# Optimization experiments

Hardware: AMD Instinct MI355X
Metric: run time of the kernel (lower is better)

The kernel has to match this reference:

```python
import jax, jax.numpy as jnp
import numpy as np

N_HEAD = 16

def setup_inputs() -> dict:
    key = jax.random.key(0)
    k1, k2, k3, k4, k5 = jax.random.split(key, 5)
    B, T, C = 2, 2048, 1024
    scale = 1.0 / np.sqrt(C)
    return {
        "x": jax.random.normal(k1, (B, T, C), dtype=jnp.float32),
        "Wqkv": jax.random.normal(k2, (C, 3 * C), dtype=jnp.float32) * scale,
        "bqkv": jax.random.normal(k3, (3 * C,), dtype=jnp.float32) * 0.02,
        "Wproj": jax.random.normal(k4, (C, C), dtype=jnp.float32) * scale,
        "bproj": jax.random.normal(k5, (C,), dtype=jnp.float32) * 0.02,
    }

def reference(x, Wqkv, bqkv, Wproj, bproj):
    B, T, C = x.shape
    H = N_HEAD
    D = C // H
    # qkv projection, split last dim as (3, H, D): first C cols = q, etc.
    qkv = (x @ Wqkv + bqkv).reshape(B, T, 3, H, D)
    q, k, v = qkv[:, :, 0], qkv[:, :, 1], qkv[:, :, 2]  # (B, T, H, D)
    att = jnp.einsum("bqhd,bkhd->bhqk", q, k) * (1.0 / np.sqrt(D))
    causal = jnp.tril(jnp.ones((T, T), dtype=bool))
    att = jnp.where(causal, att, -jnp.inf)
    att = jax.nn.softmax(att, axis=-1)
    y = jnp.einsum("bhqk,bkhd->bqhd", att, v).reshape(B, T, C)
    return y @ Wproj + bproj
```

## Files before the change

kernel.cpp:

```cpp
#include <hip/hip_runtime.h>
#include <hip/hip_bf16.h>
#include <stdint.h>

typedef unsigned short u16;
typedef __attribute__((ext_vector_type(8))) short bf16x8;
typedef __attribute__((ext_vector_type(4))) float f32x4;

#define MFMA16(a,b,c) __builtin_amdgcn_mfma_f32_16x16x32_bf16((a),(b),(c),0,0,0)

__device__ __forceinline__ u16 f2bf(float f) {
    union { float f; uint32_t u; } v; v.f = f;
    return (u16)((v.u + 0x7FFFu + ((v.u >> 16) & 1u)) >> 16);
}

__global__ void k_convert(const float* __restrict__ in, u16* __restrict__ out) {
    int i = (blockIdx.x * 256 + threadIdx.x) * 4;
    f32x4 v = *(const f32x4*)(in + i);
    uint64_t p = (uint64_t)f2bf(v[0]) | ((uint64_t)f2bf(v[1]) << 16)
               | ((uint64_t)f2bf(v[2]) << 32) | ((uint64_t)f2bf(v[3]) << 48);
    *(uint64_t*)(out + i) = p;
}

__global__ void k_transpose_convert(const float* __restrict__ W, u16* __restrict__ WT,
                                    int R, int NC) {
    int id = blockIdx.x * 256 + threadIdx.x;
    int n = id % NC, kc = id / NC;
    bf16x8 o;
#pragma unroll
    for (int i = 0; i < 8; ++i)
        o[i] = (short)f2bf(W[(size_t)(kc * 8 + i) * NC + n]);
    *(bf16x8*)(WT + (size_t)n * R + kc * 8) = o;
}

__global__ void k_transpose_v(const u16* __restrict__ V, u16* __restrict__ Vt) {
    int id = blockIdx.x * 256 + threadIdx.x;
    int d = id & 63, tc = (id >> 6) & 255, bh = id >> 14;
    const u16* src = V + (size_t)bh * 131072 + d;
    u16* dst = Vt + (size_t)bh * 131072 + (size_t)d * 2048 + tc * 8;
    bf16x8 o;
#pragma unroll
    for (int i = 0; i < 8; ++i) o[i] = (short)src[(size_t)(tc * 8 + i) * 64];
    *(bf16x8*)dst = o;
}

template<int NREP, int MODE>
__device__ __forceinline__ void gemm_body(
    const u16* __restrict__ A, const u16* __restrict__ Bt,
    const float* __restrict__ bias,
    u16* __restrict__ outQKV, float* __restrict__ outF,
    int M, int N, int K)
{
    constexpr int BN = 32 * NREP;
    constexpr int WN = 16 * NREP;
    constexpr int BSLOTS = NREP / 2;
    __shared__ __align__(16) u16 As[2][128 * 32];
    __shared__ __align__(16) u16 Bs[2][BN * 32];
    const int tid = threadIdx.x;
    const int nbx = N / BN;
    const int bm = blockIdx.x / nbx, bn = blockIdx.x % nbx;
    const int m0 = bm << 7, n0 = bn * BN;
    const int l = tid & 63, w = tid >> 6;
    const int wr = w >> 1, wc = w & 1;
    const int kl = l >> 4, lr = l & 15;

    const u16* Ag = A + (size_t)m0 * K;
    const u16* Bg = Bt + (size_t)n0 * K;

    int a_src[2], a_dst[2];
#pragma unroll
    for (int s = 0; s < 2; ++s) {
        int cb = w * 128 + s * 64;
        int c = cb + l;
        int r = c >> 2, kc = c & 3;
        a_src[s] = r * K + ((kc ^ ((r >> 1) & 3)) << 3);
        a_dst[s] = cb << 3;
    }
    int b_src[BSLOTS], b_dst[BSLOTS];
#pragma unroll
    for (int s = 0; s < BSLOTS; ++s) {
        int cb = (w * BSLOTS + s) * 64;
        int c = cb + l;
        int r = c >> 2, kc = c & 3;
        b_src[s] = r * K + ((kc ^ ((r >> 1) & 3)) << 3);
        b_dst[s] = cb << 3;
    }

    int ra[4], rb[NREP];
#pragma unroll
    for (int m = 0; m < 4; ++m) {
        int row = wr * 64 + m * 16 + lr;
        ra[m] = row * 32 + (((kl ^ (row >> 1)) & 3) << 3);
    }
#pragma unroll
    for (int n = 0; n < NREP; ++n) {
        int row = wc * WN + n * 16 + lr;
        rb[n] = row * 32 + (((kl ^ (row >> 1)) & 3) << 3);
    }

    f32x4 acc[4][NREP] = {};

#pragma unroll
    for (int s = 0; s < 2; ++s)
        __builtin_amdgcn_global_load_lds(Ag + a_src[s], &As[0][a_dst[s]], 16, 0, 0);
#pragma unroll
    for (int s = 0; s < BSLOTS; ++s)
        __builtin_amdgcn_global_load_lds(Bg + b_src[s], &Bs[0][b_dst[s]], 16, 0, 0);
    __syncthreads();

    const int nK = K >> 5;
    int cur = 0;
    for (int ks = 0; ks < nK; ++ks) {
        if (ks + 1 < nK) {
            int off = (ks + 1) << 5;
#pragma unroll
            for (int s = 0; s < 2; ++s)
                __builtin_amdgcn_global_load_lds(Ag + a_src[s] + off,
                                                 &As[cur ^ 1][a_dst[s]], 16, 0, 0);
#pragma unroll
            for (int s = 0; s < BSLOTS; ++s)
                __builtin_amdgcn_global_load_lds(Bg + b_src[s] + off,
                                                 &Bs[cur ^ 1][b_dst[s]], 16, 0, 0);
        }
        bf16x8 af[4], bfr[NREP];
#pragma unroll
        for (int m = 0; m < 4; ++m) af[m] = *(const bf16x8*)&As[cur][ra[m]];
#pragma unroll
        for (int n = 0; n < NREP; ++n) bfr[n] = *(const bf16x8*)&Bs[cur][rb[n]];
#pragma unroll
        for (int m = 0; m < 4; ++m)
#pragma unroll
            for (int n = 0; n < NREP; ++n)
                acc[m][n] = MFMA16(af[m], bfr[n], acc[m][n]);
        __syncthreads();
        cur ^= 1;
    }

    if (MODE == 0) {
#pragma unroll
        for (int n = 0; n < NREP; ++n) {
            int gn = n0 + wc * WN + n * 16 + lr;
            float bv = bias[gn];
            int s = gn >> 10, hd = gn & 1023;
            int hh = hd >> 6, dd = hd & 63;
            float mult = (s == 0) ? 0.125f : 1.0f;
            size_t base = (size_t)s * 4194304 + (size_t)hh * 131072 + dd;
#pragma unroll
            for (int m = 0; m < 4; ++m)
#pragma unroll
                for (int j = 0; j < 4; ++j) {
                    int gm = m0 + wr * 64 + m * 16 + kl * 4 + j;
                    int bb = gm >> 11, tt = gm & 2047;
                    float val = (acc[m][n][j] + bv) * mult;
                    outQKV[base + (size_t)bb * 2097152 + (size_t)tt * 64] = f2bf(val);
                }
        }
    } else {
#pragma unroll
        for (int n = 0; n < NREP; ++n) {
            int gn = n0 + wc * WN + n * 16 + lr;
            float bv = bias[gn];
#pragma unroll
            for (int m = 0; m < 4; ++m)
#pragma unroll
                for (int j = 0; j < 4; ++j) {
                    int gm = m0 + wr * 64 + m * 16 + kl * 4 + j;
                    outF[(size_t)gm * N + gn] = acc[m][n][j] + bv;
                }
        }
    }
}

__global__ __launch_bounds__(256, 4) void k_gemm_qkv(
    const u16* __restrict__ A, const u16* __restrict__ Bt,
    const float* __restrict__ bias, u16* __restrict__ outQKV,
    int M, int N, int K)
{
    gemm_body<4, 0>(A, Bt, bias, outQKV, nullptr, M, N, K);
}

__global__ __launch_bounds__(256, 4) void k_gemm_proj(
    const u16* __restrict__ A, const u16* __restrict__ Bt,
    const float* __restrict__ bias, float* __restrict__ outF,
    int M, int N, int K)
{
    gemm_body<2, 1>(A, Bt, bias, nullptr, outF, M, N, K);
}

__global__ __launch_bounds__(256, 4) void k_attn(
    const u16* __restrict__ Qg, const u16* __restrict__ Kg,
    const u16* __restrict__ Vtg, u16* __restrict__ Yg)
{
    const int bid = blockIdx.x;
    const int bh = bid & 31;
    const int qt = 31 - (bid >> 5);
    const int b = bh >> 4, h = bh & 15;
    const int q0 = qt << 6;
    const int tid = threadIdx.x, l = tid & 63, w = tid >> 6;
    const int kl = l >> 4, lr = l & 15;

    __shared__ __align__(16) u16 Qs[64 * 64];
    __shared__ __align__(16) u16 Ks[64 * 64];
    __shared__ __align__(16) u16 Vs[64 * 64];
    __shared__ __align__(16) u16 Ps[4][16 * 72];

    const u16* Qb = Qg + (size_t)bh * 131072;
    const u16* Kb = Kg + (size_t)bh * 131072;
    const u16* Vb = Vtg + (size_t)bh * 131072;

    const int rr = tid >> 3, ch = tid & 7;
    {
        bf16x8 a = *(const bf16x8*)(Qb + (size_t)(q0 + rr) * 64 + ch * 8);
        bf16x8 c = *(const bf16x8*)(Qb + (size_t)(q0 + rr + 32) * 64 + ch * 8);
        *(bf16x8*)&Qs[rr * 64 + ((ch ^ (rr & 7)) << 3)] = a;
        *(bf16x8*)&Qs[(rr + 32) * 64 + ((ch ^ (rr & 7)) << 3)] = c;
    }
    __syncthreads();
    bf16x8 qa[2];
#pragma unroll
    for (int kk = 0; kk < 2; ++kk) {
        int row = w * 16 + lr;
        qa[kk] = *(const bf16x8*)&Qs[row * 64 + (((kk * 4 + kl) ^ (row & 7)) << 3)];
    }

    f32x4 oacc[4] = {};
    float lsum[4] = {0.f, 0.f, 0.f, 0.f};

    bf16x8 kv0 = *(const bf16x8*)(Kb + (size_t)rr * 64 + ch * 8);
    bf16x8 kv1 = *(const bf16x8*)(Kb + (size_t)(rr + 32) * 64 + ch * 8);
    bf16x8 vv0 = *(const bf16x8*)(Vb + (size_t)rr * 2048 + ch * 8);
    bf16x8 vv1 = *(const bf16x8*)(Vb + (size_t)(rr + 32) * 2048 + ch * 8);

    for (int kt = 0; kt <= qt; ++kt) {
        const int k0 = kt << 6;
        __syncthreads();
        *(bf16x8*)&Ks[rr * 64 + ((ch ^ (rr & 7)) << 3)] = kv0;
        *(bf16x8*)&Ks[(rr + 32) * 64 + ((ch ^ (rr & 7)) << 3)] = kv1;
        *(bf16x8*)&Vs[rr * 64 + ((ch ^ (rr & 7)) << 3)] = vv0;
        *(bf16x8*)&Vs[(rr + 32) * 64 + ((ch ^ (rr & 7)) << 3)] = vv1;
        __syncthreads();
        if (kt < qt) {
            const int k0n = k0 + 64;
            kv0 = *(const bf16x8*)(Kb + (size_t)(k0n + rr) * 64 + ch * 8);
            kv1 = *(const bf16x8*)(Kb + (size_t)(k0n + rr + 32) * 64 + ch * 8);
            vv0 = *(const bf16x8*)(Vb + (size_t)rr * 2048 + k0n + ch * 8);
            vv1 = *(const bf16x8*)(Vb + (size_t)(rr + 32) * 2048 + k0n + ch * 8);
        }

        f32x4 s[4];
#pragma unroll
        for (int nb = 0; nb < 4; ++nb) {
            f32x4 a = {};
            int key = nb * 16 + lr;
#pragma unroll
            for (int kk = 0; kk < 2; ++kk) {
                bf16x8 kb = *(const bf16x8*)&Ks[key * 64 + (((kk * 4 + kl) ^ (key & 7)) << 3)];
                a = MFMA16(qa[kk], kb, a);
            }
            s[nb] = a;
        }
        if (kt == qt) {
#pragma unroll
            for (int nb = 0; nb < 4; ++nb) {
                int key = k0 + nb * 16 + lr;
#pragma unroll
                for (int j = 0; j < 4; ++j) {
                    int q = q0 + w * 16 + kl * 4 + j;
                    if (key > q) s[nb][j] = -__builtin_inff();
                }
            }
        }
#pragma unroll
        for (int j = 0; j < 4; ++j) {
            float acc4 = 0.f;
#pragma unroll
            for (int nb = 0; nb < 4; ++nb) {
                float p = __expf(s[nb][j]);
                s[nb][j] = p;
                acc4 += p;
            }
            lsum[j] += acc4;
        }
#pragma unroll
        for (int nb = 0; nb < 4; ++nb)
#pragma unroll
            for (int j = 0; j < 4; ++j)
                Ps[w][(kl * 4 + j) * 72 + nb * 16 + lr] = f2bf(s[nb][j]);
        bf16x8 pa[2];
#pragma unroll
        for (int kk = 0; kk < 2; ++kk)
            pa[kk] = *(const bf16x8*)&Ps[w][lr * 72 + kk * 32 + kl * 8];
#pragma unroll
        for (int db = 0; db < 4; ++db) {
            int d = db * 16 + lr;
#pragma unroll
            for (int kk = 0; kk < 2; ++kk) {
                bf16x8 vb = *(const bf16x8*)&Vs[d * 64 + (((kk * 4 + kl) ^ (d & 7)) << 3)];
                oacc[db] = MFMA16(pa[kk], vb, oacc[db]);
            }
        }
    }
#pragma unroll
    for (int j = 0; j < 4; ++j) {
#pragma unroll
        for (int off = 1; off < 16; off <<= 1) lsum[j] += __shfl_xor(lsum[j], off);
        lsum[j] = 1.f / lsum[j];
    }
#pragma unroll
    for (int db = 0; db < 4; ++db)
#pragma unroll
        for (int j = 0; j < 4; ++j) {
            int q = q0 + w * 16 + kl * 4 + j;
            int col = h * 64 + db * 16 + lr;
            Yg[(size_t)(b * 2048 + q) * 1024 + col] = f2bf(oacc[db][j] * lsum[j]);
        }
}

extern "C" void kernel_launch(void* const* d_in, const int* in_sizes, int n_in,
                              void* d_out, int out_size, void* d_ws, size_t ws_size,
                              hipStream_t stream) {
    const float* x     = (const float*)d_in[0];
    const float* Wqkv  = (const float*)d_in[1];
    const float* bqkv  = (const float*)d_in[2];
    const float* Wproj = (const float*)d_in[3];
    const float* bproj = (const float*)d_in[4];
    float* out = (float*)d_out;

    char* ws = (char*)d_ws;
    u16* xb     = (u16*)(ws);
    u16* WqkvT  = (u16*)(ws + 8388608);
    u16* WprojT = (u16*)(ws + 14680064);
    u16* qkv    = (u16*)(ws + 16777216);
    u16* Vt   = xb;
    u16* Yatt = qkv + 2 * 4194304;

    k_convert<<<4096, 256, 0, stream>>>(x, xb);
    k_transpose_convert<<<1536, 256, 0, stream>>>(Wqkv, WqkvT, 1024, 3072);
    k_transpose_convert<<<512, 256, 0, stream>>>(Wproj, WprojT, 1024, 1024);
    k_gemm_qkv<<<768, 256, 0, stream>>>(xb, WqkvT, bqkv, qkv,
                                        4096, 3072, 1024);
    k_transpose_v<<<2048, 256, 0, stream>>>(qkv + 2 * 4194304, Vt);
    k_attn<<<1024, 256, 0, stream>>>(qkv, qkv + 4194304, Vt, Yatt);
    k_gemm_proj<<<512, 256, 0, stream>>>(Yatt, WprojT, bproj, out,
                                         4096, 1024, 1024);
}
```

Measured before the change: 120.6 us.

## Triple-buffer GEMM LDS staging with counted vmcnt waits instead of syncthreads

The shared GEMM body moves from double to triple buffering of the A and B tiles in LDS. Loads now run two K-steps ahead. The full __syncthreads after each step is replaced by an s_waitcnt vmcnt that waits only for the older stage, followed by a raw s_barrier, so more global-load latency can overlap with MFMA work. The larger LDS footprint is paired with lowering the launch-bounds occupancy hint from 4 to 3 blocks, which trades some occupancy for the deeper pipeline.

```diff
diff --git a/kernel.cpp b/kernel.cpp
--- a/kernel.cpp
+++ b/kernel.cpp
@@ -53,8 +53,8 @@
     constexpr int BN = 32 * NREP;
     constexpr int WN = 16 * NREP;
     constexpr int BSLOTS = NREP / 2;
-    __shared__ __align__(16) u16 As[2][128 * 32];
-    __shared__ __align__(16) u16 Bs[2][BN * 32];
+    __shared__ __align__(16) u16 As[3][128 * 32];
+    __shared__ __align__(16) u16 Bs[3][BN * 32];
     const int tid = threadIdx.x;
     const int nbx = N / BN;
     const int bm = blockIdx.x / nbx, bn = blockIdx.x % nbx;
@@ -99,40 +99,53 @@
 
     f32x4 acc[4][NREP] = {};
 
-#pragma unroll
-    for (int s = 0; s < 2; ++s)
-        __builtin_amdgcn_global_load_lds(Ag + a_src[s], &As[0][a_dst[s]], 16, 0, 0);
-#pragma unroll
-    for (int s = 0; s < BSLOTS; ++s)
-        __builtin_amdgcn_global_load_lds(Bg + b_src[s], &Bs[0][b_dst[s]], 16, 0, 0);
-    __syncthreads();
+    auto STAGE = [&](int buf, int koff) {
+#pragma unroll
+        for (int s = 0; s < 2; ++s)
+            __builtin_amdgcn_global_load_lds(Ag + a_src[s] + koff,
+                                             &As[buf][a_dst[s]], 16, 0, 0);
+#pragma unroll
+        for (int s = 0; s < BSLOTS; ++s)
+            __builtin_amdgcn_global_load_lds(Bg + b_src[s] + koff,
+                                             &Bs[buf][b_dst[s]], 16, 0, 0);
+    };
+
+    STAGE(0, 0);
+    STAGE(1, 32);
+    if constexpr (NREP == 4) asm volatile("s_waitcnt vmcnt(4)" ::: "memory");
+    else                     asm volatile("s_waitcnt vmcnt(3)" ::: "memory");
+    __builtin_amdgcn_s_barrier();
+    __builtin_amdgcn_sched_barrier(0);
 
     const int nK = K >> 5;
-    int cur = 0;
+    int rd = 0;
     for (int ks = 0; ks < nK; ++ks) {
-        if (ks + 1 < nK) {
-            int off = (ks + 1) << 5;
-#pragma unroll
-            for (int s = 0; s < 2; ++s)
-                __builtin_amdgcn_global_load_lds(Ag + a_src[s] + off,
-                                                 &As[cur ^ 1][a_dst[s]], 16, 0, 0);
-#pragma unroll
-            for (int s = 0; s < BSLOTS; ++s)
-                __builtin_amdgcn_global_load_lds(Bg + b_src[s] + off,
-                                                 &Bs[cur ^ 1][b_dst[s]], 16, 0, 0);
+        const bool st = (ks + 2 < nK);
+        if (st) {
+            int sb = rd + 2; if (sb >= 3) sb -= 3;
+            STAGE(sb, (ks + 2) << 5);
         }
         bf16x8 af[4], bfr[NREP];
 #pragma unroll
-        for (int m = 0; m < 4; ++m) af[m] = *(const bf16x8*)&As[cur][ra[m]];
-#pragma unroll
-        for (int n = 0; n < NREP; ++n) bfr[n] = *(const bf16x8*)&Bs[cur][rb[n]];
+        for (int m = 0; m < 4; ++m) af[m] = *(const bf16x8*)&As[rd][ra[m]];
+#pragma unroll
+        for (int n = 0; n < NREP; ++n) bfr[n] = *(const bf16x8*)&Bs[rd][rb[n]];
 #pragma unroll
         for (int m = 0; m < 4; ++m)
 #pragma unroll
             for (int n = 0; n < NREP; ++n)
                 acc[m][n] = MFMA16(af[m], bfr[n], acc[m][n]);
-        __syncthreads();
-        cur ^= 1;
+        if (ks + 1 < nK) {
+            if (st) {
+                if constexpr (NREP == 4) asm volatile("s_waitcnt vmcnt(4)" ::: "memory");
+                else                     asm volatile("s_waitcnt vmcnt(3)" ::: "memory");
+            } else {
+                asm volatile("s_waitcnt vmcnt(0)" ::: "memory");
+            }
+            __builtin_amdgcn_s_barrier();
+            __builtin_amdgcn_sched_barrier(0);
+        }
+        rd = (rd == 2) ? 0 : rd + 1;
     }
 
     if (MODE == 0) {
@@ -170,7 +183,7 @@
     }
 }
 
-__global__ __launch_bounds__(256, 4) void k_gemm_qkv(
+__global__ __launch_bounds__(256, 3) void k_gemm_qkv(
     const u16* __restrict__ A, const u16* __restrict__ Bt,
     const float* __restrict__ bias, u16* __restrict__ outQKV,
     int M, int N, int K)
@@ -178,7 +191,7 @@
     gemm_body<4, 0>(A, Bt, bias, outQKV, nullptr, M, N, K);
 }
 
-__global__ __launch_bounds__(256, 4) void k_gemm_proj(
+__global__ __launch_bounds__(256, 3) void k_gemm_proj(
     const u16* __restrict__ A, const u16* __restrict__ Bt,
     const float* __restrict__ bias, float* __restrict__ outF,
     int M, int N, int K)
```

After: 121.4 us. Within noise of the previous version (+0.7%).

## Replace LDS-staged GEMM with direct global-to-register fragment loads

Applied to the files above, without the earlier changes.

Both GEMMs now skip shared memory. Each wave loads its MFMA fragments straight from global memory into registers, using a two-stage register double buffer, and no longer calls __syncthreads. The QKV GEMM tile width is halved (NREP 4 to 2) and its grid doubled so more blocks run. This removes LDS traffic and block barriers. In exchange, tiles are no longer shared between waves, so global and L2 traffic rises, and each lane reads only 16 bytes per 64-byte row segment.

```diff
diff --git a/kernel.cpp b/kernel.cpp
--- a/kernel.cpp
+++ b/kernel.cpp
@@ -44,7 +44,7 @@
 }
 
 template<int NREP, int MODE>
-__device__ __forceinline__ void gemm_body(
+__device__ __forceinline__ void gemm_direct(
     const u16* __restrict__ A, const u16* __restrict__ Bt,
     const float* __restrict__ bias,
     u16* __restrict__ outQKV, float* __restrict__ outF,
@@ -52,9 +52,6 @@
 {
     constexpr int BN = 32 * NREP;
     constexpr int WN = 16 * NREP;
-    constexpr int BSLOTS = NREP / 2;
-    __shared__ __align__(16) u16 As[2][128 * 32];
-    __shared__ __align__(16) u16 Bs[2][BN * 32];
     const int tid = threadIdx.x;
     const int nbx = N / BN;
     const int bm = blockIdx.x / nbx, bn = blockIdx.x % nbx;
@@ -63,76 +60,45 @@
     const int wr = w >> 1, wc = w & 1;
     const int kl = l >> 4, lr = l & 15;
 
-    const u16* Ag = A + (size_t)m0 * K;
-    const u16* Bg = Bt + (size_t)n0 * K;
-
-    int a_src[2], a_dst[2];
-#pragma unroll
-    for (int s = 0; s < 2; ++s) {
-        int cb = w * 128 + s * 64;
-        int c = cb + l;
-        int r = c >> 2, kc = c & 3;
-        a_src[s] = r * K + ((kc ^ ((r >> 1) & 3)) << 3);
-        a_dst[s] = cb << 3;
-    }
-    int b_src[BSLOTS], b_dst[BSLOTS];
-#pragma unroll
-    for (int s = 0; s < BSLOTS; ++s) {
-        int cb = (w * BSLOTS + s) * 64;
-        int c = cb + l;
-        int r = c >> 2, kc = c & 3;
-        b_src[s] = r * K + ((kc ^ ((r >> 1) & 3)) << 3);
-        b_dst[s] = cb << 3;
-    }
-
-    int ra[4], rb[NREP];
-#pragma unroll
-    for (int m = 0; m < 4; ++m) {
-        int row = wr * 64 + m * 16 + lr;
-        ra[m] = row * 32 + (((kl ^ (row >> 1)) & 3) << 3);
-    }
-#pragma unroll
-    for (int n = 0; n < NREP; ++n) {
-        int row = wc * WN + n * 16 + lr;
-        rb[n] = row * 32 + (((kl ^ (row >> 1)) & 3) << 3);
-    }
+    const u16* pa[4];
+#pragma unroll
+    for (int m = 0; m < 4; ++m)
+        pa[m] = A + (size_t)(m0 + wr * 64 + m * 16 + lr) * K + kl * 8;
+    const u16* pb[NREP];
+#pragma unroll
+    for (int n = 0; n < NREP; ++n)
+        pb[n] = Bt + (size_t)(n0 + wc * WN + n * 16 + lr) * K + kl * 8;
 
     f32x4 acc[4][NREP] = {};
-
-#pragma unroll
-    for (int s = 0; s < 2; ++s)
-        __builtin_amdgcn_global_load_lds(Ag + a_src[s], &As[0][a_dst[s]], 16, 0, 0);
-#pragma unroll
-    for (int s = 0; s < BSLOTS; ++s)
-        __builtin_amdgcn_global_load_lds(Bg + b_src[s], &Bs[0][b_dst[s]], 16, 0, 0);
-    __syncthreads();
+    bf16x8 a0[4], b0[NREP], a1[4], b1[NREP];
+
+#pragma unroll
+    for (int m = 0; m < 4; ++m) a0[m] = *(const bf16x8*)(pa[m]);
+#pragma unroll
+    for (int n = 0; n < NREP; ++n) b0[n] = *(const bf16x8*)(pb[n]);
 
     const int nK = K >> 5;
-    int cur = 0;
-    for (int ks = 0; ks < nK; ++ks) {
-        if (ks + 1 < nK) {
-            int off = (ks + 1) << 5;
-#pragma unroll
-            for (int s = 0; s < 2; ++s)
-                __builtin_amdgcn_global_load_lds(Ag + a_src[s] + off,
-                                                 &As[cur ^ 1][a_dst[s]], 16, 0, 0);
-#pragma unroll
-            for (int s = 0; s < BSLOTS; ++s)
-                __builtin_amdgcn_global_load_lds(Bg + b_src[s] + off,
-                                                 &Bs[cur ^ 1][b_dst[s]], 16, 0, 0);
-        }
-        bf16x8 af[4], bfr[NREP];
-#pragma unroll
-        for (int m = 0; m < 4; ++m) af[m] = *(const bf16x8*)&As[cur][ra[m]];
-#pragma unroll
-        for (int n = 0; n < NREP; ++n) bfr[n] = *(const bf16x8*)&Bs[cur][rb[n]];
+    for (int ks = 0; ks < nK; ks += 2) {
+#pragma unroll
+        for (int m = 0; m < 4; ++m) a1[m] = *(const bf16x8*)(pa[m] + (ks + 1) * 32);
+#pragma unroll
+        for (int n = 0; n < NREP; ++n) b1[n] = *(const bf16x8*)(pb[n] + (ks + 1) * 32);
 #pragma unroll
         for (int m = 0; m < 4; ++m)
 #pragma unroll
             for (int n = 0; n < NREP; ++n)
-                acc[m][n] = MFMA16(af[m], bfr[n], acc[m][n]);
-        __syncthreads();
-        cur ^= 1;
+                acc[m][n] = MFMA16(a0[m], b0[n], acc[m][n]);
+        if (ks + 2 < nK) {
+#pragma unroll
+            for (int m = 0; m < 4; ++m) a0[m] = *(const bf16x8*)(pa[m] + (ks + 2) * 32);
+#pragma unroll
+            for (int n = 0; n < NREP; ++n) b0[n] = *(const bf16x8*)(pb[n] + (ks + 2) * 32);
+        }
+#pragma unroll
+        for (int m = 0; m < 4; ++m)
+#pragma unroll
+            for (int n = 0; n < NREP; ++n)
+                acc[m][n] = MFMA16(a1[m], b1[n], acc[m][n]);
     }
 
     if (MODE == 0) {
@@ -175,7 +141,7 @@
     const float* __restrict__ bias, u16* __restrict__ outQKV,
     int M, int N, int K)
 {
-    gemm_body<4, 0>(A, Bt, bias, outQKV, nullptr, M, N, K);
+    gemm_direct<2, 0>(A, Bt, bias, outQKV, nullptr, M, N, K);
 }
 
 __global__ __launch_bounds__(256, 4) void k_gemm_proj(
@@ -183,7 +149,7 @@
     const float* __restrict__ bias, float* __restrict__ outF,
     int M, int N, int K)
 {
-    gemm_body<2, 1>(A, Bt, bias, nullptr, outF, M, N, K);
+    gemm_direct<2, 1>(A, Bt, bias, nullptr, outF, M, N, K);
 }
 
 __global__ __launch_bounds__(256, 4) void k_attn(
@@ -336,8 +302,8 @@
     k_convert<<<4096, 256, 0, stream>>>(x, xb);
     k_transpose_convert<<<1536, 256, 0, stream>>>(Wqkv, WqkvT, 1024, 3072);
     k_transpose_convert<<<512, 256, 0, stream>>>(Wproj, WprojT, 1024, 1024);
-    k_gemm_qkv<<<768, 256, 0, stream>>>(xb, WqkvT, bqkv, qkv,
-                                        4096, 3072, 1024);
+    k_gemm_qkv<<<1536, 256, 0, stream>>>(xb, WqkvT, bqkv, qkv,
+                                         4096, 3072, 1024);
     k_transpose_v<<<2048, 256, 0, stream>>>(qkv + 2 * 4194304, Vt);
     k_attn<<<1024, 256, 0, stream>>>(qkv, qkv + 4194304, Vt, Yatt);
     k_gemm_proj<<<512, 256, 0, stream>>>(Yatt, WprojT, bproj, out,
```

New measurement: 241.1 us. +100.0%, slower.
